# Performance work log

Hardware: AMD Instinct MI355X
Metric: run time of the kernel (lower is better)

The kernel has to match this reference:

```python
import jax, jax.numpy as jnp
import numpy as np
from jax import lax

IMG = 256; STRIDE = 16; FH = FW = 16; A = 9
SCALES = (32.0, 64.0, 128.0); RATIOS = (0.5, 1.0, 2.0)
N_PROP = 2000; CROP = 14
C_BB = 64


def _conv(x, w, b, stride=1, pad='SAME'):
    y = lax.conv_general_dilated(x, w, (stride, stride), pad,
                                 dimension_numbers=('NCHW', 'OIHW', 'NCHW'))
    return y + b[None, :, None, None]


def _anchors():
    s = jnp.array(SCALES, jnp.float32); r = jnp.array(RATIOS, jnp.float32)
    sr = jnp.stack(jnp.meshgrid(s, r, indexing='ij'), -1).reshape(-1, 2)  # [A,2]
    ws = sr[:, 0] * jnp.sqrt(sr[:, 1]); hs = sr[:, 0] / jnp.sqrt(sr[:, 1])
    cy = (jnp.arange(FH, dtype=jnp.float32) + 0.5) * STRIDE
    cx = (jnp.arange(FW, dtype=jnp.float32) + 0.5) * STRIDE
    cy, cx = jnp.meshgrid(cy, cx, indexing='ij')
    cy = cy[..., None]; cx = cx[..., None]  # [FH,FW,1]
    return jnp.stack([cx - ws / 2, cy - hs / 2, cx + ws / 2, cy + hs / 2], -1).reshape(-1, 4)


def _decode(deltas, anchors):
    w = anchors[:, 2] - anchors[:, 0]; h = anchors[:, 3] - anchors[:, 1]
    cx = anchors[:, 0] + 0.5 * w; cy = anchors[:, 1] + 0.5 * h
    ncx = cx + deltas[:, 0] * w; ncy = cy + deltas[:, 1] * h
    nw = w * jnp.exp(deltas[:, 2]); nh = h * jnp.exp(deltas[:, 3])
    return jnp.stack([ncx - 0.5 * nw, ncy - 0.5 * nh, ncx + 0.5 * nw, ncy + 0.5 * nh], -1)


def _clip(b):
    lim = jnp.float32(IMG - 1)
    return jnp.stack([jnp.clip(b[:, 0], 0, lim), jnp.clip(b[:, 1], 0, lim),
                      jnp.clip(b[:, 2], 0, lim), jnp.clip(b[:, 3], 0, lim)], -1)


def _nms(boxes, scores, thr):
    # greedy NMS; returns order (desc score) and keep mask in sorted order
    order = jnp.argsort(-scores)
    b = boxes[order]
    area = jnp.maximum(b[:, 2] - b[:, 0], 0) * jnp.maximum(b[:, 3] - b[:, 1], 0)
    xx1 = jnp.maximum(b[:, None, 0], b[None, :, 0]); yy1 = jnp.maximum(b[:, None, 1], b[None, :, 1])
    xx2 = jnp.minimum(b[:, None, 2], b[None, :, 2]); yy2 = jnp.minimum(b[:, None, 3], b[None, :, 3])
    inter = jnp.maximum(xx2 - xx1, 0) * jnp.maximum(yy2 - yy1, 0)
    iou = inter / (area[:, None] + area[None, :] - inter + 1e-8)
    n = boxes.shape[0]; idx = jnp.arange(n)
    def body(i, keep):
        return keep & ~(keep[i] & (iou[i] > thr) & (idx > i))
    keep = lax.fori_loop(0, n, body, jnp.ones(n, dtype=bool))
    return order, keep


def _crop_resize(feat, nboxes):
    # feat [C,FH,FW]; nboxes [N,4] normalized (y1,x1,y2,x2) -> [N,C,CROP,CROP]
    t = jnp.arange(CROP, dtype=jnp.float32) / (CROP - 1)
    def one(bx):
        y1, x1, y2, x2 = bx
        fy = (y1 + (y2 - y1) * t) * (FH - 1)
        fx = (x1 + (x2 - x1) * t) * (FW - 1)
        y0 = jnp.clip(jnp.floor(fy), 0, FH - 1).astype(jnp.int32); y1i = jnp.clip(y0 + 1, 0, FH - 1)
        x0 = jnp.clip(jnp.floor(fx), 0, FW - 1).astype(jnp.int32); x1i = jnp.clip(x0 + 1, 0, FW - 1)
        wy = (fy - y0.astype(fy.dtype))[:, None]   # [CROP,1]
        wx = (fx - x0.astype(fx.dtype))[None, :]   # [1,CROP]
        g = lambda yi, xi: feat[:, yi[:, None], xi[None, :]]  # [C,CROP,CROP]
        top = g(y0, x0) * (1 - wx) + g(y0, x1i) * wx
        bot = g(y1i, x0) * (1 - wx) + g(y1i, x1i) * wx
        return top * (1 - wy) + bot * wy
    return jax.vmap(one)(nboxes)


def _forward(x, w_bb, b_bb, w_rpn, b_rpn, w_cls, b_cls, w_box, b_box,
             w_fc1, b_fc1, w_fc2, b_fc2, w_rcls, b_rcls, w_rbox, b_rbox,
             w_m1, b_m1, w_m2, b_m2):
    anchors = _anchors()
    feat = jax.nn.relu(_conv(x, w_bb, b_bb, stride=STRIDE, pad='VALID'))  # [1,C,16,16]
    h = jax.nn.relu(_conv(feat, w_rpn, b_rpn))
    rpn_logits = _conv(h, w_cls, b_cls)[0].reshape(A, 2, FH, FW).transpose(2, 3, 0, 1).reshape(-1, 2)
    rpn_deltas = _conv(h, w_box, b_box)[0].reshape(A, 4, FH, FW).transpose(2, 3, 0, 1).reshape(-1, 4)
    scores = jax.nn.softmax(rpn_logits, -1)[:, 1]
    boxes = _clip(_decode(rpn_deltas, anchors))
    order, keep = _nms(boxes, scores, 0.5)
    n = boxes.shape[0]
    prio = jnp.where(keep, 0, 1) * n + jnp.arange(n)   # kept first, in score order
    sel = jnp.argsort(prio)[:N_PROP]
    valid = keep[sel]
    proposals = jnp.where(valid[:, None], boxes[order][sel], 0.0)  # [N_PROP,4] xyxy
    nb = jnp.stack([proposals[:, 1], proposals[:, 0], proposals[:, 3], proposals[:, 2]], -1) / (IMG - 1)
    crops = _crop_resize(feat[0], nb)                  # [N_PROP,C,14,14]
    pooled = crops.reshape(N_PROP, C_BB, 7, 2, 7, 2).max(axis=(3, 5))
    flat = pooled.reshape(N_PROP, -1)
    h1 = jax.nn.relu(flat @ w_fc1 + b_fc1)
    h2 = jax.nn.relu(h1 @ w_fc2 + b_fc2)
    rcnn_logits = h2 @ w_rcls + b_rcls                 # [N_PROP,2]
    rcnn_deltas = h2 @ w_rbox + b_rbox                 # [N_PROP,4]
    m = jax.nn.relu(_conv(crops, w_m1, b_m1))
    rcnn_masks = _conv(m, w_m2, b_m2)                  # [N_PROP,1,14,14]
    det_scores = jax.nn.softmax(rcnn_logits, -1)[:, 1]
    dets = _clip(_decode(rcnn_deltas, proposals))
    s2 = jnp.where(valid, det_scores, -1.0)
    order2, keep2 = _nms(dets, s2, 0.3)
    keep2 = keep2 & valid[order2]
    final_dets = jnp.where(keep2[:, None], dets[order2], 0.0)
    final_scores = jnp.where(keep2, det_scores[order2], 0.0)
    final_masks = jax.nn.sigmoid(rcnn_masks[order2][:, 0]) * keep2[:, None, None].astype(crops.dtype)
    return (rpn_logits, rpn_deltas, proposals, anchors, rcnn_logits, rcnn_deltas,
            rcnn_masks, final_dets, final_masks, final_scores, keep2)


def setup_inputs() -> dict:
    key = jax.random.key(0)
    ks = jax.random.split(key, 24)
    rn = lambda k, sh, s: jax.random.normal(k, sh, dtype=jnp.float32) * s
    C = C_BB
    return {
        'x': rn(ks[0], (1, 3, IMG, IMG), 1.0),
        'w_bb': rn(ks[1], (C, 3, STRIDE, STRIDE), 0.03), 'b_bb': jnp.zeros((C,), jnp.float32),
        'w_rpn': rn(ks[2], (C, C, 3, 3), 0.05), 'b_rpn': jnp.zeros((C,), jnp.float32),
        'w_cls': rn(ks[3], (2 * A, C, 1, 1), 0.05), 'b_cls': jnp.zeros((2 * A,), jnp.float32),
        'w_box': rn(ks[4], (4 * A, C, 1, 1), 0.05), 'b_box': jnp.zeros((4 * A,), jnp.float32),
        'w_fc1': rn(ks[5], (C * 7 * 7, 512), 0.02), 'b_fc1': jnp.zeros((512,), jnp.float32),
        'w_fc2': rn(ks[6], (512, 512), 0.04), 'b_fc2': jnp.zeros((512,), jnp.float32),
        'w_rcls': rn(ks[7], (512, 2), 0.05), 'b_rcls': jnp.zeros((2,), jnp.float32),
        'w_rbox': rn(ks[8], (512, 4), 0.05), 'b_rbox': jnp.zeros((4,), jnp.float32),
        'w_m1': rn(ks[9], (C, C, 3, 3), 0.05), 'b_m1': jnp.zeros((C,), jnp.float32),
        'w_m2': rn(ks[10], (1, C, 1, 1), 0.05), 'b_m2': jnp.zeros((1,), jnp.float32),
    }


def reference(x, w_bb, b_bb, w_rpn, b_rpn, w_cls, b_cls, w_box, b_box,
              w_fc1, b_fc1, w_fc2, b_fc2, w_rcls, b_rcls, w_rbox, b_rbox,
              w_m1, b_m1, w_m2, b_m2):
    return _forward(x, w_bb, b_bb, w_rpn, b_rpn, w_cls, b_cls, w_box, b_box,
                    w_fc1, b_fc1, w_fc2, b_fc2, w_rcls, b_rcls, w_rbox, b_rbox,
                    w_m1, b_m1, w_m2, b_m2)
```

## Files before the change

kernel.cpp:

```cpp
#include <hip/hip_runtime.h>
#include <math.h>

typedef unsigned long long u64;
typedef unsigned short u16;
typedef __attribute__((ext_vector_type(8))) short bf16x8;
typedef __attribute__((ext_vector_type(4))) float f32x4;
typedef __attribute__((ext_vector_type(16))) float f32x16;

#define N_ANCH 2304
#define NP     2000
#define W1     36
#define W2     32

#define O_RPN_LOGITS   0
#define O_RPN_DELTAS   4608
#define O_PROPOSALS    13824
#define O_ANCHORS      21824
#define O_RCNN_LOGITS  31040
#define O_RCNN_DELTAS  35040
#define O_RCNN_MASKS   43040
#define O_FINAL_DETS   435040
#define O_FINAL_MASKS  443040
#define O_FINAL_SCORES 835040
#define O_KEEP2        837040

__device__ __forceinline__ u16 f2bf(float f) {
    unsigned int x = __float_as_uint(f);
    unsigned int r = x + 0x7fffu + ((x >> 16) & 1u);
    return (u16)(r >> 16);
}

__global__ __launch_bounds__(256) void bb_conv(const float* __restrict__ x,
    const float* __restrict__ w, const float* __restrict__ b,
    float* __restrict__ feat, float* __restrict__ feat_tf)
{
    __shared__ __align__(16) float ws_[768];
    int c = blockIdx.x;
    for (int e = threadIdx.x; e < 192; e += 256)
        ((float4*)ws_)[e] = ((const float4*)(w + c*768))[e];
    __syncthreads();
    int fy = threadIdx.x >> 4, fx = threadIdx.x & 15;
    float acc = b[c];
    for (int ic = 0; ic < 3; ++ic)
        for (int ky = 0; ky < 16; ++ky) {
            const float* xr = x + (size_t)(ic*256 + fy*16+ky)*256 + fx*16;
            const float* wr = ws_ + ic*256 + ky*16;
            float xv[16];
            *(float4*)&xv[0]  = *(const float4*)(xr);
            *(float4*)&xv[4]  = *(const float4*)(xr+4);
            *(float4*)&xv[8]  = *(const float4*)(xr+8);
            *(float4*)&xv[12] = *(const float4*)(xr+12);
            #pragma unroll
            for (int kx = 0; kx < 16; ++kx) acc += xv[kx]*wr[kx];
        }
    float v = fmaxf(acc, 0.f);
    feat[c*256 + threadIdx.x] = v;
    feat_tf[threadIdx.x*64 + c] = v;
}

__global__ __launch_bounds__(256) void rpn_conv(const float* __restrict__ feat,
    const float* __restrict__ w, const float* __restrict__ b, float* __restrict__ h)
{
    __shared__ __align__(16) float f[16384];
    __shared__ __align__(16) float ws_[576];
    int c = blockIdx.x;
    for (int e = threadIdx.x; e < 4096; e += 256)
        ((float4*)f)[e] = ((const float4*)feat)[e];
    for (int e = threadIdx.x; e < 144; e += 256)
        ((float4*)ws_)[e] = ((const float4*)(w + c*576))[e];
    __syncthreads();
    int fy = threadIdx.x >> 4, fx = threadIdx.x & 15;
    float acc = b[c];
    for (int ic = 0; ic < 64; ++ic) {
        const float* fc = f + ic*256;
        const float* wc = ws_ + ic*9;
        #pragma unroll
        for (int dy = 0; dy < 3; ++dy) {
            int y = fy + dy - 1;
            if (y < 0 || y > 15) continue;
            #pragma unroll
            for (int dx = 0; dx < 3; ++dx) {
                int xx = fx + dx - 1;
                if (xx < 0 || xx > 15) continue;
                acc += fc[y*16+xx]*wc[dy*3+dx];
            }
        }
    }
    h[c*256 + threadIdx.x] = fmaxf(acc, 0.f);
}

__global__ __launch_bounds__(256) void heads_rpn(const float* __restrict__ hbuf,
    const float* __restrict__ w_cls, const float* __restrict__ b_cls,
    const float* __restrict__ w_box, const float* __restrict__ b_box,
    float* __restrict__ out_logits, float* __restrict__ out_deltas,
    float* __restrict__ out_anchors,
    float* __restrict__ scores, float* __restrict__ boxes)
{
    int idx = blockIdx.x*256 + threadIdx.x;
    if (idx >= N_ANCH) return;
    int fy = idx / 144, r = idx % 144, fx = r / 9, a = r % 9;
    int pix = fy*16 + fx;
    float l0 = b_cls[a*2+0], l1 = b_cls[a*2+1];
    float d0 = b_box[a*4+0], d1 = b_box[a*4+1], d2 = b_box[a*4+2], d3 = b_box[a*4+3];
    const float* wc0 = w_cls + (a*2+0)*64;
    const float* wc1 = w_cls + (a*2+1)*64;
    const float* wb0 = w_box + (a*4+0)*64;
    const float* wb1 = w_box + (a*4+1)*64;
    const float* wb2 = w_box + (a*4+2)*64;
    const float* wb3 = w_box + (a*4+3)*64;
    for (int c = 0; c < 64; ++c) {
        float hv = hbuf[c*256 + pix];
        l0 += hv*wc0[c]; l1 += hv*wc1[c];
        d0 += hv*wb0[c]; d1 += hv*wb1[c]; d2 += hv*wb2[c]; d3 += hv*wb3[c];
    }
    out_logits[idx*2+0] = l0; out_logits[idx*2+1] = l1;
    out_deltas[idx*4+0] = d0; out_deltas[idx*4+1] = d1;
    out_deltas[idx*4+2] = d2; out_deltas[idx*4+3] = d3;
    float mx = fmaxf(l0,l1);
    float e0 = expf(l0-mx), e1 = expf(l1-mx);
    scores[idx] = e1/(e0+e1);
    float SC = (a/3 == 0) ? 32.f : ((a/3 == 1) ? 64.f : 128.f);
    float RT = (a%3 == 0) ? 0.5f : ((a%3 == 1) ? 1.f : 2.f);
    float wsz = SC*sqrtf(RT), hsz = SC/sqrtf(RT);
    float cx = (fx+0.5f)*16.f, cy = (fy+0.5f)*16.f;
    float ax1 = cx - wsz*0.5f, ay1 = cy - hsz*0.5f;
    float ax2 = cx + wsz*0.5f, ay2 = cy + hsz*0.5f;
    out_anchors[idx*4+0]=ax1; out_anchors[idx*4+1]=ay1;
    out_anchors[idx*4+2]=ax2; out_anchors[idx*4+3]=ay2;
    float aw = ax2-ax1, ah = ay2-ay1;
    float acx = ax1 + 0.5f*aw, acy = ay1 + 0.5f*ah;
    float ncx = acx + d0*aw, ncy = acy + d1*ah;
    float nw = aw*expf(d2), nh = ah*expf(d3);
    float x1 = ncx - 0.5f*nw, y1 = ncy - 0.5f*nh;
    float x2 = ncx + 0.5f*nw, y2 = ncy + 0.5f*nh;
    const float lim = 255.f;
    x1 = fminf(fmaxf(x1,0.f),lim); y1 = fminf(fmaxf(y1,0.f),lim);
    x2 = fminf(fmaxf(x2,0.f),lim); y2 = fminf(fmaxf(y2,0.f),lim);
    boxes[idx*4+0]=x1; boxes[idx*4+1]=y1; boxes[idx*4+2]=x2; boxes[idx*4+3]=y2;
}

__global__ __launch_bounds__(256) void rank_part(const float* __restrict__ score,
    int* __restrict__ parts, int n)
{
    __shared__ __align__(16) float sj[256];
    int it = blockIdx.x, jt = blockIdx.y;
    int i = it*256 + threadIdx.x;
    int j0 = jt*256;
    int jj = j0 + threadIdx.x;
    sj[threadIdx.x] = (jj < n) ? score[jj] : 0.f;
    __syncthreads();
    if (i >= n) return;
    float si = score[i];
    int jmax = min(256, n - j0);
    int cnt = 0;
    const float4* s4 = (const float4*)sj;
    int q4 = jmax >> 2;
    for (int q = 0; q < q4; ++q) {
        float4 v = s4[q];
        int j = j0 + q*4;
        cnt += (v.x > si) || (v.x == si && (j+0) < i);
        cnt += (v.y > si) || (v.y == si && (j+1) < i);
        cnt += (v.z > si) || (v.z == si && (j+2) < i);
        cnt += (v.w > si) || (v.w == si && (j+3) < i);
    }
    parts[(size_t)jt*n + i] = cnt;
}

__global__ __launch_bounds__(256) void rank_scatter(const int* __restrict__ parts,
    int* __restrict__ order, int n, int S)
{
    int i = blockIdx.x*256 + threadIdx.x;
    if (i >= n) return;
    int r = 0;
    for (int s = 0; s < S; ++s) r += parts[(size_t)s*n + i];
    order[r] = i;
}

__global__ __launch_bounds__(256) void gather_sorted(const float4* __restrict__ boxes,
    const int* __restrict__ order, float4* __restrict__ sb, float* __restrict__ sa, int n)
{
    int i = blockIdx.x*256 + threadIdx.x;
    if (i >= n) return;
    float4 b = boxes[order[i]];
    sb[i] = b;
    sa[i] = fmaxf(b.z-b.x, 0.f)*fmaxf(b.w-b.y, 0.f);
}

__global__ __launch_bounds__(256) void iou_mask(const float4* __restrict__ sb,
    const float* __restrict__ sa, int n, int ntotal, int words, float thr,
    u64* __restrict__ mask)
{
    int gid = blockIdx.x*256 + threadIdx.x;
    if (gid >= ntotal*words) return;
    int i = gid / words, w = gid % words;
    if (i >= n) { mask[(size_t)i*words + w] = 0; return; }
    float4 bi = sb[i]; float ai = sa[i];
    u64 m = 0;
    int j0 = w*64;
    for (int bb = 0; bb < 64; ++bb) {
        int j = j0 + bb;
        if (j > i && j < n) {
            float4 bj = sb[j];
            float xx1 = fmaxf(bi.x, bj.x), yy1 = fmaxf(bi.y, bj.y);
            float xx2 = fminf(bi.z, bj.z), yy2 = fminf(bi.w, bj.w);
            float inter = fmaxf(xx2-xx1, 0.f)*fmaxf(yy2-yy1, 0.f);
            float iou = inter / (ai + sa[j] - inter + 1e-8f);
            if (iou > thr) m |= 1ULL << bb;
        }
    }
    mask[(size_t)i*words + w] = m;
}

__global__ __launch_bounds__(256, 1) void nms_scan_wg(const u64* __restrict__ mask,
    int nblk, int words, u64* __restrict__ remout)
{
    __shared__ u64 rem_lds[64];
    __shared__ u64 diagS[64];
    __shared__ u64 pslot[8*64];
    int t = threadIdx.x;
    int ngrp = 256 / words;
    int g = t / words, c = t % words;
    bool pactive = (g < ngrp);
    int gg = min(g, ngrp - 1);
    if (t < 64) {
        rem_lds[t] = ~0ULL;
        diagS[t] = mask[(size_t)t*words + 0];
    }
    __syncthreads();
    for (int b = 0; b < nblk; ++b) {
        const u64* blockbase = mask + (size_t)(64*b)*words;
        u64 vals[10];
        int rows[10];
        #pragma unroll
        for (int k = 0; k < 10; ++k) {
            int r = min(gg + k*ngrp, 63);
            rows[k] = r;
            vals[k] = blockbase[(size_t)r*words + c];
        }
        u64 dnext = mask[(size_t)(64*(b+1) + (t & 63))*words + min(b+1, words-1)];
        u64 mydia = diagS[t & 63];
        u64 nz = __ballot(mydia != 0ULL);
        u64 cur = rem_lds[b];
        u64 pend = cur & nz;
        unsigned mlo = (unsigned)mydia;
        unsigned mhi = (unsigned)(mydia >> 32);
        while (pend) {
            int i = __ffsll((unsigned long long)pend) - 1;
            unsigned lo = __builtin_amdgcn_readlane((int)mlo, i);
            unsigned hi = __builtin_amdgcn_readlane((int)mhi, i);
            u64 dia = ((u64)hi << 32) | lo;
            cur  &= ~dia;
            pend &= ~dia;
            pend &= pend - 1;
        }
        u64 partial = ~0ULL;
        #pragma unroll
        for (int k = 0; k < 10; ++k) {
            bool al = (cur >> rows[k]) & 1ULL;
            partial &= al ? ~vals[k] : ~0ULL;
        }
        if (pactive) pslot[g*64 + c] = partial;
        __syncthreads();
        if (t < 64) diagS[t] = dnext;
        if (t < words) {
            u64 red = rem_lds[t];
            for (int g2 = 0; g2 < ngrp; ++g2) red &= pslot[g2*64 + t];
            rem_lds[t] = red;
        }
        __syncthreads();
    }
    if (t < words) remout[t] = rem_lds[t];
}

__global__ __launch_bounds__(256) void select_props(const u64* __restrict__ remw,
    const float4* __restrict__ sboxes, float* __restrict__ prop_out,
    float4* __restrict__ propws, int* __restrict__ validat, int* __restrict__ kcnt)
{
    __shared__ int cnt[256];
    __shared__ int pref[257];
    int t = threadIdx.x;
    int base = t*9;
    int c = 0;
    #pragma unroll
    for (int q = 0; q < 9; ++q) { int i = base+q; c += (int)((remw[i>>6]>>(i&63))&1ULL); }
    cnt[t] = c; __syncthreads();
    if (t == 0) { pref[0]=0; for (int u=0;u<256;u++) pref[u+1]=pref[u]+cnt[u]; }
    __syncthreads();
    int K = pref[256];
    if (t == 0) kcnt[0] = K;
    int kb = pref[t];
    int nb = K + (base - pref[t]);
    for (int q = 0; q < 9; ++q) {
        int i = base + q;
        int k = (int)((remw[i>>6]>>(i&63))&1ULL);
        int pos = k ? kb : nb;
        if (k) kb++; else nb++;
        if (pos < NP) {
            validat[pos] = k;
            float4 p = k ? sboxes[i] : make_float4(0.f,0.f,0.f,0.f);
            propws[pos] = p;
            prop_out[pos*4+0]=p.x; prop_out[pos*4+1]=p.y;
            prop_out[pos*4+2]=p.z; prop_out[pos*4+3]=p.w;
        }
    }
}

__global__ __launch_bounds__(256) void prep_wbt(const float* __restrict__ w, u16* __restrict__ wbt)
{
    int e = blockIdx.x*256 + threadIdx.x;
    if (e >= 36864) return;
    int oc = e / 576, rem = e % 576, ic = rem / 9, tap = rem % 9;
    int kg = ic >> 4, half = (ic >> 3) & 1, el = ic & 7;
    wbt[((tap*4 + kg)*2 + half)*512 + oc*8 + el] = f2bf(w[e]);
}

__global__ __launch_bounds__(256, 3) void mask_head_fused(const float* __restrict__ feat_tf,
    const float4* __restrict__ propws, const u16* __restrict__ wbt,
    const float* __restrict__ b_m1, const float* __restrict__ w_m2,
    const float* __restrict__ b_m2, float* __restrict__ masks_out,
    float* __restrict__ flat, const int* __restrict__ kcnt)
{
    __shared__ __align__(16) u16 crop[256*64];
    __shared__ unsigned pooled[3136];
    __shared__ __align__(16) int4 cidx[196];
    __shared__ float2 cwt[196];
    __shared__ int2 cmeta[196];
    __shared__ __align__(16) float wm2s[64];
    __shared__ __align__(16) float b1s[64];
    int n = blockIdx.x;
    if (n > *kcnt) return;
    int t = threadIdx.x;
    float4 p = propws[n];

    #pragma unroll
    for (int k = 0; k < 8; ++k)
        *(int4*)(crop + k*2048 + t*8) = make_int4(0,0,0,0);
    for (int e = t; e < 3136; e += 256) pooled[e] = 0;
    if (t < 64) { wm2s[t] = w_m2[t]; b1s[t] = b_m1[t]; }
    if (t < 196) {
        float x1n = p.x*(1.f/255.f), y1n = p.y*(1.f/255.f);
        float x2n = p.z*(1.f/255.f), y2n = p.w*(1.f/255.f);
        int py = t / 14, px = t - py*14;
        float fyv = (y1n + (y2n-y1n)*(py*(1.f/13.f)))*15.f;
        float fxv = (x1n + (x2n-x1n)*(px*(1.f/13.f)))*15.f;
        int y0 = min(max((int)floorf(fyv),0),15), y1i = min(y0+1,15);
        int x0 = min(max((int)floorf(fxv),0),15), x1i = min(x0+1,15);
        float wy = fyv - (float)y0, wx = fxv - (float)x0;
        cidx[t] = make_int4((y0*16+x0)*64, (y0*16+x1i)*64, (y1i*16+x0)*64, (y1i*16+x1i)*64);
        cwt[t] = make_float2(wy, wx);
        cmeta[t] = make_int2((py+1)*16 + px + 1, (py>>1)*7 + (px>>1));
    }
    __syncthreads();

    int wave = t >> 6, lane = t & 63;
    for (int it = 0; it < 49; ++it) {
        int idx = it*4 + wave;
        int4 o4 = cidx[idx];
        float2 w2 = cwt[idx];
        int2 mt = cmeta[idx];
        float v00 = feat_tf[o4.x + lane];
        float v01 = feat_tf[o4.y + lane];
        float v10 = feat_tf[o4.z + lane];
        float v11 = feat_tf[o4.w + lane];
        float wy = w2.x, wx = w2.y;
        float top = v00*(1.f-wx) + v01*wx;
        float bot = v10*(1.f-wx) + v11*wx;
        float val = top*(1.f-wy) + bot*wy;
        int g = mt.x;
        crop[g*64 + (((lane>>3) ^ (g&7))<<3) + (lane&7)] = f2bf(val);
        atomicMax(&pooled[lane*49 + mt.y], __float_as_uint(val));
    }
    __syncthreads();

    {
        size_t rowoff = (size_t)n*3136;
        for (int k = t; k < 3136; k += 256)
            flat[rowoff + k] = __uint_as_float(pooled[k]);
    }

    int l31 = lane & 31, half = lane >> 5;
    int pix0 = wave*64 + l31, pix1 = pix0 + 32;

    f32x16 acc[2][2];
    #pragma unroll
    for (int o = 0; o < 2; ++o) {
        #pragma unroll
        for (int q = 0; q < 4; ++q) {
            float4 b4 = *(const float4*)&b1s[o*32 + 4*half + 8*q];
            #pragma unroll
            for (int pp = 0; pp < 2; ++pp) {
                acc[pp][o][q*4+0] = b4.x; acc[pp][o][q*4+1] = b4.y;
                acc[pp][o][q*4+2] = b4.z; acc[pp][o][q*4+3] = b4.w;
            }
        }
    }

    for (int tap = 0; tap < 9; ++tap) {
        int doff = (tap/3 - 1)*16 + (tap%3) - 1;
        int p0 = (pix0 + doff) & 255;
        int p1 = (pix1 + doff) & 255;
        const u16* wt = wbt + tap*4096;
        bf16x8 af[2][4];
        #pragma unroll
        for (int kg = 0; kg < 4; ++kg) {
            #pragma unroll
            for (int o = 0; o < 2; ++o)
                af[o][kg] = *(const bf16x8*)(wt + (kg*2 + half)*512 + (o*32 + l31)*8);
        }
        int x0v = p0&7, x1v = p1&7;
        #pragma unroll
        for (int kg = 0; kg < 4; ++kg) {
            int slot = kg*2 + half;
            bf16x8 bf0 = *(const bf16x8*)(crop + p0*64 + ((slot ^ x0v)<<3));
            bf16x8 bf1 = *(const bf16x8*)(crop + p1*64 + ((slot ^ x1v)<<3));
            acc[0][0] = __builtin_amdgcn_mfma_f32_32x32x16_bf16(af[0][kg], bf0, acc[0][0], 0, 0, 0);
            acc[0][1] = __builtin_amdgcn_mfma_f32_32x32x16_bf16(af[1][kg], bf0, acc[0][1], 0, 0, 0);
            acc[1][0] = __builtin_amdgcn_mfma_f32_32x32x16_bf16(af[0][kg], bf1, acc[1][0], 0, 0, 0);
            acc[1][1] = __builtin_amdgcn_mfma_f32_32x32x16_bf16(af[1][kg], bf1, acc[1][1], 0, 0, 0);
        }
    }

    float4 wmq[2][4];
    #pragma unroll
    for (int o = 0; o < 2; ++o)
        #pragma unroll
        for (int q = 0; q < 4; ++q)
            wmq[o][q] = *(const float4*)&wm2s[o*32 + 4*half + 8*q];
    float s0 = 0.f, s1 = 0.f;
    #pragma unroll
    for (int o = 0; o < 2; ++o) {
        #pragma unroll
        for (int q = 0; q < 4; ++q) {
            float4 w4 = wmq[o][q];
            s0 = fmaf(fmaxf(acc[0][o][q*4+0], 0.f), w4.x, s0);
            s0 = fmaf(fmaxf(acc[0][o][q*4+1], 0.f), w4.y, s0);
            s0 = fmaf(fmaxf(acc[0][o][q*4+2], 0.f), w4.z, s0);
            s0 = fmaf(fmaxf(acc[0][o][q*4+3], 0.f), w4.w, s0);
            s1 = fmaf(fmaxf(acc[1][o][q*4+0], 0.f), w4.x, s1);
            s1 = fmaf(fmaxf(acc[1][o][q*4+1], 0.f), w4.y, s1);
            s1 = fmaf(fmaxf(acc[1][o][q*4+2], 0.f), w4.z, s1);
            s1 = fmaf(fmaxf(acc[1][o][q*4+3], 0.f), w4.w, s1);
        }
    }
    s0 += __shfl_xor(s0, 32);
    s1 += __shfl_xor(s1, 32);
    float sv = (half ? s1 : s0) + b_m2[0];
    int pw = half ? pix1 : pix0;
    int pyy = (pw>>4) - 1, pxx = (pw&15) - 1;
    if ((unsigned)pyy < 14u && (unsigned)pxx < 14u)
        masks_out[(size_t)n*196 + pyy*14 + pxx] = sv;
}

__global__ __launch_bounds__(256) void bcast_rows(const int* __restrict__ kcnt,
    float* __restrict__ out_logits, float* __restrict__ out_deltas,
    float* __restrict__ masks_out, float4* __restrict__ dets,
    float* __restrict__ dscores, float* __restrict__ s2)
{
    int K = *kcnt;
    int j = blockIdx.x;
    if (j <= K) return;
    int t = threadIdx.x;
    if (t < 196) {
        masks_out[(size_t)j*196 + t] = masks_out[(size_t)K*196 + t];
    } else if (t == 196) {
        out_logits[j*2+0] = out_logits[K*2+0];
        out_logits[j*2+1] = out_logits[K*2+1];
    } else if (t == 197) {
        out_deltas[j*4+0] = out_deltas[K*4+0];
        out_deltas[j*4+1] = out_deltas[K*4+1];
        out_deltas[j*4+2] = out_deltas[K*4+2];
        out_deltas[j*4+3] = out_deltas[K*4+3];
    } else if (t == 198) {
        dets[j] = dets[K];
        dscores[j] = dscores[K];
        s2[j] = s2[K];
    }
}

__global__ __launch_bounds__(128) void gemm_f32_t32(const float* __restrict__ A,
    const float* __restrict__ B, float* __restrict__ Cpart,
    int M, int N, int K, int Kblk, const int* __restrict__ kcnt)
{
    int row0 = blockIdx.x*32, col0 = blockIdx.y*64;
    if (row0 > *kcnt) return;
    __shared__ float As[32][36];
    __shared__ float Bs[32][68];
    int s = blockIdx.z;
    int kbase = s*Kblk;
    int t = threadIdx.x;

    int arow = t >> 2;
    int ak   = (t & 3) * 8;
    int am = min(row0 + arow, M-1);
    const float* Arow = A + (size_t)am*K + kbase;
    int bk = t >> 2;
    int bc = (t & 3) * 16;
    const float* Bbase = B + (size_t)(kbase + bk)*N + col0 + bc;

    int wv = t >> 6, lane = t & 63;
    int cx = lane & 15;
    int ry = lane >> 4;
    int rbase = wv*16 + ry*4;
    int cxx = cx*4;

    float4 pa0 = *(const float4*)(Arow + ak);
    float4 pa1 = *(const float4*)(Arow + ak + 4);
    float4 pb0 = *(const float4*)(Bbase);
    float4 pb1 = *(const float4*)(Bbase + 4);
    float4 pb2 = *(const float4*)(Bbase + 8);
    float4 pb3 = *(const float4*)(Bbase + 12);

    float acc[4][4] = {};
    for (int k0 = 0; k0 < Kblk; k0 += 32) {
        As[ak+0][arow]=pa0.x; As[ak+1][arow]=pa0.y; As[ak+2][arow]=pa0.z; As[ak+3][arow]=pa0.w;
        As[ak+4][arow]=pa1.x; As[ak+5][arow]=pa1.y; As[ak+6][arow]=pa1.z; As[ak+7][arow]=pa1.w;
        *(float4*)&Bs[bk][bc]    = pb0;
        *(float4*)&Bs[bk][bc+4]  = pb1;
        *(float4*)&Bs[bk][bc+8]  = pb2;
        *(float4*)&Bs[bk][bc+12] = pb3;
        __syncthreads();
        int kn = k0 + 32;
        if (kn < Kblk) {
            pa0 = *(const float4*)(Arow + kn + ak);
            pa1 = *(const float4*)(Arow + kn + ak + 4);
            pb0 = *(const float4*)(Bbase + (size_t)kn*N);
            pb1 = *(const float4*)(Bbase + (size_t)kn*N + 4);
            pb2 = *(const float4*)(Bbase + (size_t)kn*N + 8);
            pb3 = *(const float4*)(Bbase + (size_t)kn*N + 12);
        }
        #pragma unroll
        for (int k = 0; k < 32; ++k) {
            float4 av = *(float4*)&As[k][rbase];
            float4 bv = *(float4*)&Bs[k][cxx];
            float a_[4] = {av.x, av.y, av.z, av.w};
            float b_[4] = {bv.x, bv.y, bv.z, bv.w};
            #pragma unroll
            for (int i = 0; i < 4; ++i)
                #pragma unroll
                for (int j = 0; j < 4; ++j)
                    acc[i][j] = fmaf(a_[i], b_[j], acc[i][j]);
        }
        __syncthreads();
    }
    float* Cp = Cpart + (size_t)s*M*N;
    #pragma unroll
    for (int i = 0; i < 4; ++i) {
        int gm = row0 + rbase + i;
        if (gm >= M) continue;
        #pragma unroll
        for (int j = 0; j < 4; ++j) {
            int gn = col0 + cxx + j;
            Cp[(size_t)gm*N + gn] = acc[i][j];
        }
    }
}

__global__ __launch_bounds__(256) void combine_parts(const float* __restrict__ parts,
    const float* __restrict__ bias, float* __restrict__ C,
    int MN, int N, int S, int relu, const int* __restrict__ kcnt)
{
    int i4 = blockIdx.x*256 + threadIdx.x;
    if (i4*4 >= MN) return;
    size_t idx = (size_t)i4*4;
    if ((int)(idx / (unsigned)N) > *kcnt) return;
    float4 acc = *(const float4*)(parts + idx);
    for (int s = 1; s < S; ++s) {
        float4 v = *(const float4*)(parts + (size_t)s*MN + idx);
        acc.x += v.x; acc.y += v.y; acc.z += v.z; acc.w += v.w;
    }
    int nb = (int)(idx & (N-1));
    float4 bv = *(const float4*)(bias + nb);
    acc.x += bv.x; acc.y += bv.y; acc.z += bv.z; acc.w += bv.w;
    if (relu) {
        acc.x = fmaxf(acc.x, 0.f); acc.y = fmaxf(acc.y, 0.f);
        acc.z = fmaxf(acc.z, 0.f); acc.w = fmaxf(acc.w, 0.f);
    }
    *(float4*)(C + idx) = acc;
}

__global__ __launch_bounds__(256) void rcnn_heads_lds(const float* __restrict__ h2,
    const float* __restrict__ w_rcls, const float* __restrict__ b_rcls,
    const float* __restrict__ w_rbox, const float* __restrict__ b_rbox,
    const float4* __restrict__ propws, const int* __restrict__ validat,
    float* __restrict__ out_logits, float* __restrict__ out_deltas,
    float4* __restrict__ dets, float* __restrict__ dscores, float* __restrict__ s2,
    const int* __restrict__ kcnt)
{
    int b0 = blockIdx.x*8;
    if (b0 > *kcnt) return;
    __shared__ float hs[8*520];
    for (int e = threadIdx.x; e < 8*512; e += 256) {
        int pr = e >> 9, k = e & 511;
        hs[pr*520 + k] = h2[(size_t)(b0+pr)*512 + k];
    }
    __syncthreads();
    int t = threadIdx.x;
    if (t >= 8) return;
    int n = b0 + t;
    const float* hv = hs + t*520;
    float l0 = b_rcls[0], l1 = b_rcls[1];
    float d0 = b_rbox[0], d1 = b_rbox[1], d2 = b_rbox[2], d3 = b_rbox[3];
    for (int k = 0; k < 512; ++k) {
        float v = hv[k];
        l0 = fmaf(v, w_rcls[k*2+0], l0); l1 = fmaf(v, w_rcls[k*2+1], l1);
        d0 = fmaf(v, w_rbox[k*4+0], d0); d1 = fmaf(v, w_rbox[k*4+1], d1);
        d2 = fmaf(v, w_rbox[k*4+2], d2); d3 = fmaf(v, w_rbox[k*4+3], d3);
    }
    out_logits[n*2+0]=l0; out_logits[n*2+1]=l1;
    out_deltas[n*4+0]=d0; out_deltas[n*4+1]=d1;
    out_deltas[n*4+2]=d2; out_deltas[n*4+3]=d3;
    float mx = fmaxf(l0,l1);
    float e0 = expf(l0-mx), e1 = expf(l1-mx);
    float sc = e1/(e0+e1);
    float4 p = propws[n];
    float w = p.z-p.x, h = p.w-p.y;
    float cx = p.x + 0.5f*w, cy = p.y + 0.5f*h;
    float ncx = cx + d0*w, ncy = cy + d1*h;
    float nw = w*expf(d2), nh = h*expf(d3);
    float x1 = ncx-0.5f*nw, y1 = ncy-0.5f*nh, x2 = ncx+0.5f*nw, y2 = ncy+0.5f*nh;
    const float lim = 255.f;
    x1 = fminf(fmaxf(x1,0.f),lim); y1 = fminf(fmaxf(y1,0.f),lim);
    x2 = fminf(fmaxf(x2,0.f),lim); y2 = fminf(fmaxf(y2,0.f),lim);
    dets[n] = make_float4(x1,y1,x2,y2);
    dscores[n] = sc;
    s2[n] = validat[n] ? sc : -1.0f;
}

__global__ void finalize(const u64* __restrict__ remw2,
    const int* __restrict__ order2, const int* __restrict__ validat,
    const float4* __restrict__ dets, const float* __restrict__ dscores,
    const float* __restrict__ masks_in, float* __restrict__ fdets,
    float* __restrict__ fscores, float* __restrict__ fmasks, float* __restrict__ keep2out)
{
    int j = blockIdx.x;
    int t = threadIdx.x;
    int o = order2[j];
    int kb = (int)((remw2[j>>6] >> (j&63)) & 1ULL);
    int k2 = kb & validat[o];
    if (t == 0) {
        float4 d = dets[o];
        if (!k2) d = make_float4(0.f,0.f,0.f,0.f);
        fdets[j*4+0]=d.x; fdets[j*4+1]=d.y; fdets[j*4+2]=d.z; fdets[j*4+3]=d.w;
        fscores[j] = k2 ? dscores[o] : 0.f;
        keep2out[j] = (float)k2;
    }
    if (t < 196) {
        float mv = masks_in[(size_t)o*196 + t];
        float sg = 1.f/(1.f + expf(-mv));
        fmasks[(size_t)j*196 + t] = k2 ? sg : 0.f;
    }
}

extern "C" void kernel_launch(void* const* d_in, const int* in_sizes, int n_in,
                              void* d_out, int out_size, void* d_ws, size_t ws_size,
                              hipStream_t stream)
{
    const float* x      = (const float*)d_in[0];
    const float* w_bb   = (const float*)d_in[1];
    const float* b_bb   = (const float*)d_in[2];
    const float* w_rpn  = (const float*)d_in[3];
    const float* b_rpn  = (const float*)d_in[4];
    const float* w_cls  = (const float*)d_in[5];
    const float* b_cls  = (const float*)d_in[6];
    const float* w_box  = (const float*)d_in[7];
    const float* b_box  = (const float*)d_in[8];
    const float* w_fc1  = (const float*)d_in[9];
    const float* b_fc1  = (const float*)d_in[10];
    const float* w_fc2  = (const float*)d_in[11];
    const float* b_fc2  = (const float*)d_in[12];
    const float* w_rcls = (const float*)d_in[13];
    const float* b_rcls = (const float*)d_in[14];
    const float* w_rbox = (const float*)d_in[15];
    const float* b_rbox = (const float*)d_in[16];
    const float* w_m1   = (const float*)d_in[17];
    const float* b_m1   = (const float*)d_in[18];
    const float* w_m2   = (const float*)d_in[19];
    const float* b_m2   = (const float*)d_in[20];

    float* out = (float*)d_out;

    char* basep = (char*)d_ws;
    auto alloc = [&](size_t bytes) { char* q = basep; basep += (bytes + 255) & ~(size_t)255; return q; };
    float* feat    = (float*)alloc(16384*4);
    float* feat_tf = (float*)alloc(16384*4);
    float* hbuf    = (float*)alloc(16384*4);
    float* scores  = (float*)alloc(2304*4);
    float* boxes   = (float*)alloc(9216*4);
    int*   order1  = (int*)  alloc(2304*4);
    int*   rparts  = (int*)  alloc((size_t)9*2304*4);
    float* sboxes  = (float*)alloc(9216*4);
    float* sareas  = (float*)alloc(2304*4);
    u64*   supm1   = (u64*)  alloc((size_t)((W1+1)*64)*W1*8);
    u64*   remw1   = (u64*)  alloc(W1*8);
    int*   validat = (int*)  alloc(NP*4);
    float* propws  = (float*)alloc(NP*4*4);
    int*   kcnt    = (int*)  alloc(4);
    u16*   wbt     = (u16*)  alloc(36864*2);
    float* flat    = (float*)alloc((size_t)NP*3136*4);
    float* h1      = (float*)alloc((size_t)NP*512*4);
    float* h2      = (float*)alloc((size_t)NP*512*4);
    float* gparts  = (float*)alloc((size_t)7*NP*512*4);
    float* dets    = (float*)alloc(NP*4*4);
    float* dscores = (float*)alloc(NP*4);
    float* s2      = (float*)alloc(NP*4);
    int*   order2  = (int*)  alloc(NP*4);
    float* sdets   = (float*)alloc(NP*4*4);
    float* sareas2 = (float*)alloc(NP*4);
    u64*   supm2   = (u64*)  alloc((size_t)((W2+1)*64)*W2*8);
    u64*   remw2   = (u64*)  alloc(W2*8);

    bb_conv<<<64, 256, 0, stream>>>(x, w_bb, b_bb, feat, feat_tf);
    rpn_conv<<<64, 256, 0, stream>>>(feat, w_rpn, b_rpn, hbuf);
    heads_rpn<<<9, 256, 0, stream>>>(hbuf, w_cls, b_cls, w_box, b_box,
        out + O_RPN_LOGITS, out + O_RPN_DELTAS, out + O_ANCHORS, scores, boxes);

    rank_part<<<dim3(9, 9), 256, 0, stream>>>(scores, rparts, N_ANCH);
    rank_scatter<<<9, 256, 0, stream>>>(rparts, order1, N_ANCH, 9);
    gather_sorted<<<9, 256, 0, stream>>>((const float4*)boxes, order1,
                                         (float4*)sboxes, sareas, N_ANCH);
    iou_mask<<<(W1*64*W1+255)/256, 256, 0, stream>>>((const float4*)sboxes, sareas,
                                                     N_ANCH, W1*64, W1, 0.5f, supm1);
    nms_scan_wg<<<1, 256, 0, stream>>>(supm1, W1, W1, remw1);
    select_props<<<1, 256, 0, stream>>>(remw1, (const float4*)sboxes,
                                        out + O_PROPOSALS, (float4*)propws, validat, kcnt);

    prep_wbt<<<144, 256, 0, stream>>>(w_m1, wbt);

    mask_head_fused<<<NP, 256, 0, stream>>>(feat_tf, (const float4*)propws, wbt,
        b_m1, w_m2, b_m2, out + O_RCNN_MASKS, flat, kcnt);
    gemm_f32_t32<<<dim3(63, 8, 7), 128, 0, stream>>>(flat, w_fc1, gparts,
                                                     NP, 512, 3136, 448, kcnt);
    combine_parts<<<(NP*512/4+255)/256, 256, 0, stream>>>(gparts, b_fc1, h1,
                                                          NP*512, 512, 7, 1, kcnt);
    gemm_f32_t32<<<dim3(63, 8, 2), 128, 0, stream>>>(h1, w_fc2, gparts,
                                                     NP, 512, 512, 256, kcnt);
    combine_parts<<<(NP*512/4+255)/256, 256, 0, stream>>>(gparts, b_fc2, h2,
                                                          NP*512, 512, 2, 1, kcnt);
    rcnn_heads_lds<<<250, 256, 0, stream>>>(h2, w_rcls, b_rcls, w_rbox, b_rbox,
        (const float4*)propws, validat, out + O_RCNN_LOGITS, out + O_RCNN_DELTAS,
        (float4*)dets, dscores, s2, kcnt);

    bcast_rows<<<NP, 256, 0, stream>>>(kcnt, out + O_RCNN_LOGITS, out + O_RCNN_DELTAS,
        out + O_RCNN_MASKS, (float4*)dets, dscores, s2);

    rank_part<<<dim3(8, 8), 256, 0, stream>>>(s2, rparts, NP);
    rank_scatter<<<8, 256, 0, stream>>>(rparts, order2, NP, 8);
    gather_sorted<<<8, 256, 0, stream>>>((const float4*)dets, order2,
                                         (float4*)sdets, sareas2, NP);
    iou_mask<<<(W2*64*W2+255)/256, 256, 0, stream>>>((const float4*)sdets, sareas2,
                                                     NP, W2*64, W2, 0.3f, supm2);
    nms_scan_wg<<<1, 256, 0, stream>>>(supm2, W2, W2, remw2);
    finalize<<<NP, 256, 0, stream>>>(remw2, order2, validat, (const float4*)dets,
        dscores, out + O_RCNN_MASKS, out + O_FINAL_DETS, out + O_FINAL_SCORES,
        out + O_FINAL_MASKS, out + O_KEEP2);
}
```

Before: 448.3 us.

## Replace LDS-tiled FC GEMM with register-only direct-load GEMM

The fp32 split-K GEMM for the two FC layers no longer stages A and B tiles through shared memory with barriers. Each thread now loads its own four A rows and four B rows straight from global memory, four k-steps at a time, prefetching the next step in registers. This removes LDS traffic and __syncthreads, but drops data sharing inside the block, so every thread issues many more global loads and leans on the cache for reuse.

Measured after the change: 524.2 us. +16.9%, slower.

```diff
diff --git a/kernel.cpp b/kernel.cpp
--- a/kernel.cpp
+++ b/kernel.cpp
@@ -477,70 +477,70 @@
     }
 }
 
-__global__ __launch_bounds__(128) void gemm_f32_t32(const float* __restrict__ A,
+__global__ __launch_bounds__(128) void gemm_f32_reg(const float* __restrict__ A,
     const float* __restrict__ B, float* __restrict__ Cpart,
     int M, int N, int K, int Kblk, const int* __restrict__ kcnt)
 {
     int row0 = blockIdx.x*32, col0 = blockIdx.y*64;
     if (row0 > *kcnt) return;
-    __shared__ float As[32][36];
-    __shared__ float Bs[32][68];
     int s = blockIdx.z;
     int kbase = s*Kblk;
     int t = threadIdx.x;
-
-    int arow = t >> 2;
-    int ak   = (t & 3) * 8;
-    int am = min(row0 + arow, M-1);
-    const float* Arow = A + (size_t)am*K + kbase;
-    int bk = t >> 2;
-    int bc = (t & 3) * 16;
-    const float* Bbase = B + (size_t)(kbase + bk)*N + col0 + bc;
-
     int wv = t >> 6, lane = t & 63;
     int cx = lane & 15;
     int ry = lane >> 4;
     int rbase = wv*16 + ry*4;
     int cxx = cx*4;
 
-    float4 pa0 = *(const float4*)(Arow + ak);
-    float4 pa1 = *(const float4*)(Arow + ak + 4);
-    float4 pb0 = *(const float4*)(Bbase);
-    float4 pb1 = *(const float4*)(Bbase + 4);
-    float4 pb2 = *(const float4*)(Bbase + 8);
-    float4 pb3 = *(const float4*)(Bbase + 12);
+    const float* Ar0 = A + (size_t)min(row0 + rbase + 0, M-1)*K + kbase;
+    const float* Ar1 = A + (size_t)min(row0 + rbase + 1, M-1)*K + kbase;
+    const float* Ar2 = A + (size_t)min(row0 + rbase + 2, M-1)*K + kbase;
+    const float* Ar3 = A + (size_t)min(row0 + rbase + 3, M-1)*K + kbase;
+    const float* Bp  = B + (size_t)kbase*N + col0 + cxx;
+
+    float4 a0 = *(const float4*)(Ar0);
+    float4 a1 = *(const float4*)(Ar1);
+    float4 a2 = *(const float4*)(Ar2);
+    float4 a3 = *(const float4*)(Ar3);
+    float4 b0 = *(const float4*)(Bp);
+    float4 b1 = *(const float4*)(Bp + (size_t)N);
+    float4 b2 = *(const float4*)(Bp + (size_t)2*N);
+    float4 b3 = *(const float4*)(Bp + (size_t)3*N);
 
     float acc[4][4] = {};
-    for (int k0 = 0; k0 < Kblk; k0 += 32) {
-        As[ak+0][arow]=pa0.x; As[ak+1][arow]=pa0.y; As[ak+2][arow]=pa0.z; As[ak+3][arow]=pa0.w;
-        As[ak+4][arow]=pa1.x; As[ak+5][arow]=pa1.y; As[ak+6][arow]=pa1.z; As[ak+7][arow]=pa1.w;
-        *(float4*)&Bs[bk][bc]    = pb0;
-        *(float4*)&Bs[bk][bc+4]  = pb1;
-        *(float4*)&Bs[bk][bc+8]  = pb2;
-        *(float4*)&Bs[bk][bc+12] = pb3;
-        __syncthreads();
-        int kn = k0 + 32;
-        if (kn < Kblk) {
-            pa0 = *(const float4*)(Arow + kn + ak);
-            pa1 = *(const float4*)(Arow + kn + ak + 4);
-            pb0 = *(const float4*)(Bbase + (size_t)kn*N);
-            pb1 = *(const float4*)(Bbase + (size_t)kn*N + 4);
-            pb2 = *(const float4*)(Bbase + (size_t)kn*N + 8);
-            pb3 = *(const float4*)(Bbase + (size_t)kn*N + 12);
-        }
-        #pragma unroll
-        for (int k = 0; k < 32; ++k) {
-            float4 av = *(float4*)&As[k][rbase];
-            float4 bv = *(float4*)&Bs[k][cxx];
-            float a_[4] = {av.x, av.y, av.z, av.w};
-            float b_[4] = {bv.x, bv.y, bv.z, bv.w};
+    for (int c = 0; c < Kblk; c += 4) {
+        float4 an0, an1, an2, an3, bn0, bn1, bn2, bn3;
+        int cn = c + 4;
+        if (cn < Kblk) {
+            an0 = *(const float4*)(Ar0 + cn);
+            an1 = *(const float4*)(Ar1 + cn);
+            an2 = *(const float4*)(Ar2 + cn);
+            an3 = *(const float4*)(Ar3 + cn);
+            const float* Bn = Bp + (size_t)cn*N;
+            bn0 = *(const float4*)(Bn);
+            bn1 = *(const float4*)(Bn + (size_t)N);
+            bn2 = *(const float4*)(Bn + (size_t)2*N);
+            bn3 = *(const float4*)(Bn + (size_t)3*N);
+        }
+        float av[4][4] = {{a0.x,a1.x,a2.x,a3.x},
+                          {a0.y,a1.y,a2.y,a3.y},
+                          {a0.z,a1.z,a2.z,a3.z},
+                          {a0.w,a1.w,a2.w,a3.w}};
+        float bv[4][4] = {{b0.x,b0.y,b0.z,b0.w},
+                          {b1.x,b1.y,b1.z,b1.w},
+                          {b2.x,b2.y,b2.z,b2.w},
+                          {b3.x,b3.y,b3.z,b3.w}};
+        #pragma unroll
+        for (int kk = 0; kk < 4; ++kk)
             #pragma unroll
             for (int i = 0; i < 4; ++i)
                 #pragma unroll
                 for (int j = 0; j < 4; ++j)
-                    acc[i][j] = fmaf(a_[i], b_[j], acc[i][j]);
-        }
-        __syncthreads();
+                    acc[i][j] = fmaf(av[kk][i], bv[kk][j], acc[i][j]);
+        if (cn < Kblk) {
+            a0 = an0; a1 = an1; a2 = an2; a3 = an3;
+            b0 = bn0; b1 = bn1; b2 = bn2; b3 = bn3;
+        }
     }
     float* Cp = Cpart + (size_t)s*M*N;
     #pragma unroll
@@ -728,11 +728,11 @@
 
     mask_head_fused<<<NP, 256, 0, stream>>>(feat_tf, (const float4*)propws, wbt,
         b_m1, w_m2, b_m2, out + O_RCNN_MASKS, flat, kcnt);
-    gemm_f32_t32<<<dim3(63, 8, 7), 128, 0, stream>>>(flat, w_fc1, gparts,
+    gemm_f32_reg<<<dim3(63, 8, 7), 128, 0, stream>>>(flat, w_fc1, gparts,
                                                      NP, 512, 3136, 448, kcnt);
     combine_parts<<<(NP*512/4+255)/256, 256, 0, stream>>>(gparts, b_fc1, h1,
                                                           NP*512, 512, 7, 1, kcnt);
-    gemm_f32_t32<<<dim3(63, 8, 2), 128, 0, stream>>>(h1, w_fc2, gparts,
+    gemm_f32_reg<<<dim3(63, 8, 2), 128, 0, stream>>>(h1, w_fc2, gparts,
                                                      NP, 512, 512, 256, kcnt);
     combine_parts<<<(NP*512/4+255)/256, 256, 0, stream>>>(gparts, b_fc2, h2,
                                                           NP*512, 512, 2, 1, kcnt);
```
